# Kernel optimization log

Hardware: AMD Instinct MI355X
Metric: run time of the kernel (lower is better)

Reference implementation:

```python
import jax, jax.numpy as jnp
import numpy as np

NUM_EMBED = 1024
EMBED_DIM = 256
DECAY = 0.99
EPS = 1e-05
COMMIT = 0.25


def setup_inputs() -> dict:
    key = jax.random.key(0)
    k1, k2, k3 = jax.random.split(key, 3)
    z = jax.random.normal(k1, (64, 32, 32, EMBED_DIM), dtype=jnp.float32)
    lim = 1.0 / NUM_EMBED
    embeddings = jax.random.uniform(k2, (NUM_EMBED, EMBED_DIM), minval=-lim, maxval=lim, dtype=jnp.float32)
    ema_embed = jax.random.uniform(k3, (NUM_EMBED, EMBED_DIM), minval=-lim, maxval=lim, dtype=jnp.float32)
    cluster_size = jnp.zeros((NUM_EMBED,), dtype=jnp.float32)
    return {"z": z, "embeddings": embeddings, "ema_embed": ema_embed, "cluster_size": cluster_size}


def reference(z, embeddings, ema_embed, cluster_size):
    B, H, W, D = z.shape
    zf = z.reshape(-1, D)  # [N, D]
    # squared euclidean distances to codebook: [N, K]
    distances = (zf ** 2).sum(-1, keepdims=True) + (embeddings ** 2).sum(-1) - 2.0 * (zf @ embeddings.T)
    closest = jnp.argmin(distances, axis=-1)  # [N] int
    quantized_indices = closest.reshape(B, H, W)[:, None]  # [B,1,H,W]
    quantized = embeddings[closest].reshape(z.shape)  # gather instead of one-hot GEMM

    # --- training-mode EMA codebook update (buffer math, no grads) ---
    n_i = jnp.zeros((NUM_EMBED,), dtype=zf.dtype).at[closest].add(1.0)  # per-code counts
    new_cluster = cluster_size * DECAY + n_i * (1.0 - DECAY)
    dw = jnp.zeros_like(embeddings).at[closest].add(zf)  # scatter-add of assigned vectors
    new_ema = ema_embed * DECAY + dw * (1.0 - DECAY)
    n = new_cluster.sum()
    new_cluster = (new_cluster + EPS) / (n + NUM_EMBED * EPS) * n
    new_embeddings = new_ema / new_cluster[:, None]

    commitment_loss = jnp.mean((quantized - z) ** 2)
    st_quantized = z + jax.lax.stop_gradient(quantized - z)  # straight-through
    loss = commitment_loss * COMMIT
    return loss, st_quantized, quantized_indices, new_embeddings, new_cluster, new_ema
```

## Files before the change

### kernel.cpp

```cpp
#include <hip/hip_runtime.h>
#include <float.h>
#include <stdint.h>

#define K_EMB 1024
#define D_EMB 256

typedef _Float16 half8 __attribute__((ext_vector_type(8)));
typedef float f32x4_t __attribute__((ext_vector_type(4)));

typedef const __attribute__((address_space(1))) void* as1cv;
typedef __attribute__((address_space(3))) void* as3v;


__global__ void convert_e_kernel(const float* __restrict__ e, _Float16* __restrict__ ehp,
                                 float* __restrict__ t2, unsigned int* __restrict__ flag_cnt) {
  if (blockIdx.x == 0 && threadIdx.x == 0) { flag_cnt[0] = 0; flag_cnt[1] = 0; }
  int row = blockIdx.x * 4 + (threadIdx.x >> 6);
  int lane = threadIdx.x & 63;
  float4 v = ((const float4*)(e + (size_t)row * D_EMB))[lane];
  float s = v.x * v.x + v.y * v.y + v.z * v.z + v.w * v.w;
#pragma unroll
  for (int off = 32; off > 0; off >>= 1) s += __shfl_down(s, off, 64);
  if (lane == 0) t2[row] = s;
  _Float16* dst = ehp + (size_t)row * D_EMB + lane * 4;
  dst[0] = (_Float16)v.x; dst[1] = (_Float16)v.y;
  dst[2] = (_Float16)v.z; dst[3] = (_Float16)v.w;
}


#define BM 128
#define CCH 32
#define NCH (K_EMB / CCH)
#define DELTA 1.5e-4f

__launch_bounds__(256, 3)
__global__ void argmin_mfma_kernel(const float* __restrict__ z,
                                   const _Float16* __restrict__ eh,
                                   const float* __restrict__ t2,
                                   int* __restrict__ closest,
                                   float* __restrict__ idx_out,
                                   unsigned int* __restrict__ flag_cnt,
                                   unsigned int* __restrict__ flag_row,
                                   unsigned int* __restrict__ flag_cand) {
  __shared__ _Float16 ebuf[3][CCH * D_EMB];
  const int tid = threadIdx.x;
  const int wid = tid >> 6;
  const int lane = tid & 63;
  const int c = lane & 15, g = lane >> 4;
  const int row0 = blockIdx.x * BM + wid * 32;

  half8 A[2][8];
#pragma unroll
  for (int fr = 0; fr < 2; ++fr)
#pragma unroll
    for (int df = 0; df < 8; ++df) {
      const float* zp = z + (size_t)(row0 + fr * 16 + c) * D_EMB + df * 32 + g * 8;
      const float4 v0 = *(const float4*)zp;
      const float4 v1 = *(const float4*)(zp + 4);
      half8 h;
      h[0] = (_Float16)v0.x; h[1] = (_Float16)v0.y; h[2] = (_Float16)v0.z; h[3] = (_Float16)v0.w;
      h[4] = (_Float16)v1.x; h[5] = (_Float16)v1.y; h[6] = (_Float16)v1.z; h[7] = (_Float16)v1.w;
      A[fr][df] = h;
    }

  float m1[8], m2[8], m3[8];
  int k1[8], k2[8];
#pragma unroll
  for (int s = 0; s < 8; ++s) { m1[s] = FLT_MAX; m2[s] = FLT_MAX; m3[s] = FLT_MAX; k1[s] = 0; k2[s] = 0; }

#define INS(s, dvv, kkv)                                        \
  {                                                             \
    const float dv_ = (dvv); const int kk_ = (kkv);             \
    const bool lt1 = dv_ < m1[s];                               \
    const bool lt2 = dv_ < m2[s];                               \
    m3[s] = __builtin_amdgcn_fmed3f(m2[s], m3[s], dv_);         \
    const float nm2 = __builtin_amdgcn_fmed3f(m1[s], m2[s], dv_); \
    k2[s] = lt1 ? k1[s] : (lt2 ? kk_ : k2[s]);                  \
    m2[s] = nm2;                                                \
    m1[s] = fminf(m1[s], dv_);                                  \
    k1[s] = lt1 ? kk_ : k1[s];                                  \
  }

  const int rswz = (c & 7) << 3;

  int sgs[4];
#pragma unroll
  for (int u = 0; u < 4; ++u) {
    const int gidx = (wid * 4 + u) * 64 + lane;
    sgs[u] = (gidx & ~7) | ((gidx & 7) ^ ((gidx >> 5) & 7));
  }

#define ISSUE(cbn, buf)                                                              \
  {                                                                                  \
    const _Float16* src_ = eh + (size_t)(cbn) * (CCH * D_EMB);                       \
    _Float16* db_ = &ebuf[buf][0];                                                   \
    _Pragma("unroll")                                                                \
    for (int u = 0; u < 4; ++u)                                                      \
      __builtin_amdgcn_global_load_lds((as1cv)(src_ + (size_t)sgs[u] * 8),           \
                                       (as3v)(db_ + (wid * 4 + u) * 512), 16, 0, 0); \
  }

#define COMPUTE(rb_, cb_)                                                            \
  {                                                                                  \
    f32x4_t acc[2][2];                                                               \
    _Pragma("unroll")                                                                \
    for (int fr = 0; fr < 2; ++fr)                                                   \
      _Pragma("unroll")                                                              \
      for (int fc = 0; fc < 2; ++fc) acc[fr][fc] = (f32x4_t){0.f, 0.f, 0.f, 0.f};    \
    _Pragma("unroll")                                                                \
    for (int d = 0; d < 8; ++d) {                                                    \
      half8 Bh[2];                                                                   \
      _Pragma("unroll")                                                              \
      for (int fc = 0; fc < 2; ++fc) {                                               \
        const int elem = (d * 32 + g * 8) ^ rswz;                                    \
        Bh[fc] = *(const half8*)(&ebuf[rb_][(fc * 16 + c) * D_EMB + elem]);          \
      }                                                                              \
      _Pragma("unroll")                                                              \
      for (int fr = 0; fr < 2; ++fr)                                                 \
        _Pragma("unroll")                                                            \
        for (int fc = 0; fc < 2; ++fc)                                               \
          acc[fr][fc] = __builtin_amdgcn_mfma_f32_16x16x32_f16(A[fr][d], Bh[fc],     \
                                                               acc[fr][fc], 0, 0, 0);\
    }                                                                                \
    _Pragma("unroll")                                                                \
    for (int fc = 0; fc < 2; ++fc) {                                                 \
      const int kk = (cb_)*CCH + fc * 16 + c;                                        \
      const float t2c = t2[kk];                                                      \
      _Pragma("unroll")                                                              \
      for (int fr = 0; fr < 2; ++fr)                                                 \
        _Pragma("unroll")                                                            \
        for (int r = 0; r < 4; ++r) {                                                \
          const float dv = fmaf(-2.f, acc[fr][fc][r], t2c);                          \
          const int s = fr * 4 + r;                                                  \
          INS(s, dv, kk)                                                             \
        }                                                                            \
    }                                                                                \
  }

  ISSUE(0, 0)
  ISSUE(1, 1)

  for (int cb = 0; cb < NCH - 1; ++cb) {
    asm volatile("s_waitcnt vmcnt(4)" ::: "memory");
    __builtin_amdgcn_s_barrier();
    __builtin_amdgcn_sched_barrier(0);
    if (cb + 2 < NCH) ISSUE(cb + 2, (cb + 2) % 3)
    const int rb = cb % 3;
    COMPUTE(rb, cb)
  }
  asm volatile("s_waitcnt vmcnt(0)" ::: "memory");
  __builtin_amdgcn_s_barrier();
  __builtin_amdgcn_sched_barrier(0);
  {
    const int rb = (NCH - 1) % 3;
    COMPUTE(rb, NCH - 1)
  }
#undef COMPUTE
#undef ISSUE

#pragma unroll
  for (int m = 1; m <= 8; m <<= 1) {
#pragma unroll
    for (int s = 0; s < 8; ++s) {
      const float om1 = __shfl_xor(m1[s], m, 64);
      const int ok1 = __shfl_xor(k1[s], m, 64);
      const float om2 = __shfl_xor(m2[s], m, 64);
      const int ok2 = __shfl_xor(k2[s], m, 64);
      const float om3 = __shfl_xor(m3[s], m, 64);
      INS(s, om1, ok1)
      INS(s, om2, ok2)
      m3[s] = fminf(m3[s], om3);
    }
  }
#undef INS

  if (c == 0) {
#pragma unroll
    for (int s = 0; s < 8; ++s) {
      const int fr = s >> 2, r = s & 3;
      const int row = row0 + fr * 16 + g * 4 + r;
      closest[row] = k1[s];
      idx_out[row] = (float)k1[s];
      if (m2[s] - m1[s] < DELTA) {
        const unsigned int p = atomicAdd(flag_cnt, 1u);
        flag_row[p] = (unsigned int)row;
        flag_cand[p] = (unsigned int)k1[s] | ((unsigned int)k2[s] << 10) |
                       ((m3[s] - m1[s] < DELTA) ? (1u << 20) : 0u);
      }
    }
  }
}


__launch_bounds__(256, 4)
__global__ void fixup_pair_kernel(const float* __restrict__ z, const float* __restrict__ emb,
                                  const float* __restrict__ t2,
                                  const unsigned int* __restrict__ flag_cnt,
                                  const unsigned int* __restrict__ flag_row,
                                  const unsigned int* __restrict__ flag_cand,
                                  int* __restrict__ closest, float* __restrict__ idx_out,
                                  unsigned int* __restrict__ flag2_cnt,
                                  unsigned int* __restrict__ flag2) {
  const int tid = threadIdx.x;
  const int q = tid & 3;
  const unsigned int cnt = *flag_cnt;
  const unsigned int nquads = (gridDim.x * 256) >> 2;
  for (unsigned int i = (blockIdx.x * 256 + tid) >> 2; i < cnt; i += nquads) {
    const int row = (int)flag_row[i];
    const unsigned int cand = flag_cand[i];
    if ((cand >> 20) & 1u) {
      if (q == 0) {
        const unsigned int p = atomicAdd(flag2_cnt, 1u);
        flag2[p] = (unsigned int)row;
      }
      continue;
    }
    const int ka = (int)(cand & 1023u), kb = (int)((cand >> 10) & 1023u);
    const float4* zp = (const float4*)(z + (size_t)row * D_EMB) + q * 16;
    const float4* ap = (const float4*)(emb + (size_t)ka * D_EMB) + q * 16;
    const float4* bp = (const float4*)(emb + (size_t)kb * D_EMB) + q * 16;
    float s0 = 0.f, sa = 0.f, sb = 0.f;
#pragma unroll 8
    for (int u = 0; u < 16; ++u) {
      const float4 zv = zp[u], av = ap[u], bv = bp[u];
      s0 = fmaf(zv.x, zv.x, s0); s0 = fmaf(zv.y, zv.y, s0);
      s0 = fmaf(zv.z, zv.z, s0); s0 = fmaf(zv.w, zv.w, s0);
      sa = fmaf(zv.x, av.x, sa); sa = fmaf(zv.y, av.y, sa);
      sa = fmaf(zv.z, av.z, sa); sa = fmaf(zv.w, av.w, sa);
      sb = fmaf(zv.x, bv.x, sb); sb = fmaf(zv.y, bv.y, sb);
      sb = fmaf(zv.z, bv.z, sb); sb = fmaf(zv.w, bv.w, sb);
    }
#pragma unroll
    for (int m = 1; m <= 2; m <<= 1) {
      s0 += __shfl_xor(s0, m, 64);
      sa += __shfl_xor(sa, m, 64);
      sb += __shfl_xor(sb, m, 64);
    }
    if (q == 0) {
      const float da = (s0 + t2[ka]) - 2.f * sa;
      const float db = (s0 + t2[kb]) - 2.f * sb;
      int kbest = ka;
      if (db < da || (db == da && kb < ka)) kbest = kb;
      closest[row] = kbest;
      idx_out[row] = (float)kbest;
    }
  }
}


__launch_bounds__(256, 4)
__global__ void fixup_full_kernel(const float* __restrict__ z, const float* __restrict__ emb,
                                  const float* __restrict__ t2,
                                  const unsigned int* __restrict__ flag2_cnt,
                                  const unsigned int* __restrict__ flag2,
                                  int* __restrict__ closest, float* __restrict__ idx_out) {
  __shared__ float zs[D_EMB];
  __shared__ float t1s;
  __shared__ float redm[4];
  __shared__ int redk[4];
  const int tid = threadIdx.x;
  const int lane = tid & 63, wv = tid >> 6;
  const unsigned int cnt = *flag2_cnt;
  for (unsigned int j = blockIdx.x; j < cnt; j += gridDim.x) {
    __syncthreads();
    const int row = (int)flag2[j];
    if (wv == 0) {
      const float4 v = ((const float4*)(z + (size_t)row * D_EMB))[lane];
      ((float4*)zs)[lane] = v;
      float s = v.x * v.x + v.y * v.y + v.z * v.z + v.w * v.w;
#pragma unroll
      for (int off = 32; off > 0; off >>= 1) s += __shfl_down(s, off, 64);
      if (lane == 0) t1s = s;
    }
    __syncthreads();
    const float4* e0 = (const float4*)(emb + (size_t)(4 * tid + 0) * D_EMB);
    const float4* e1 = (const float4*)(emb + (size_t)(4 * tid + 1) * D_EMB);
    const float4* e2 = (const float4*)(emb + (size_t)(4 * tid + 2) * D_EMB);
    const float4* e3 = (const float4*)(emb + (size_t)(4 * tid + 3) * D_EMB);
    const float4* zp4 = (const float4*)zs;
    float a0 = 0.f, a1 = 0.f, a2 = 0.f, a3 = 0.f;
    for (int i = 0; i < 64; ++i) {
      const float4 z4 = zp4[i];
      const float4 v0 = e0[i], v1 = e1[i], v2 = e2[i], v3 = e3[i];
      a0 = fmaf(z4.x, v0.x, a0); a0 = fmaf(z4.y, v0.y, a0);
      a0 = fmaf(z4.z, v0.z, a0); a0 = fmaf(z4.w, v0.w, a0);
      a1 = fmaf(z4.x, v1.x, a1); a1 = fmaf(z4.y, v1.y, a1);
      a1 = fmaf(z4.z, v1.z, a1); a1 = fmaf(z4.w, v1.w, a1);
      a2 = fmaf(z4.x, v2.x, a2); a2 = fmaf(z4.y, v2.y, a2);
      a2 = fmaf(z4.z, v2.z, a2); a2 = fmaf(z4.w, v2.w, a2);
      a3 = fmaf(z4.x, v3.x, a3); a3 = fmaf(z4.y, v3.y, a3);
      a3 = fmaf(z4.z, v3.z, a3); a3 = fmaf(z4.w, v3.w, a3);
    }
    const float t1v = t1s;
    float best = FLT_MAX;
    int bk = 0x7fffffff;
    const float dvs[4] = {(t1v + t2[4 * tid + 0]) - 2.f * a0,
                          (t1v + t2[4 * tid + 1]) - 2.f * a1,
                          (t1v + t2[4 * tid + 2]) - 2.f * a2,
                          (t1v + t2[4 * tid + 3]) - 2.f * a3};
#pragma unroll
    for (int cc = 0; cc < 4; ++cc) {
      const int k = 4 * tid + cc;
      if (dvs[cc] < best) { best = dvs[cc]; bk = k; }
    }
#pragma unroll
    for (int m = 1; m <= 32; m <<= 1) {
      const float ob = __shfl_xor(best, m, 64);
      const int ok = __shfl_xor(bk, m, 64);
      if (ob < best || (ob == best && ok < bk)) { best = ob; bk = ok; }
    }
    if (lane == 0) { redm[wv] = best; redk[wv] = bk; }
    __syncthreads();
    if (tid == 0) {
      float b = redm[0];
      int k = redk[0];
#pragma unroll
      for (int w = 1; w < 4; ++w)
        if (redm[w] < b || (redm[w] == b && redk[w] < k)) { b = redm[w]; k = redk[w]; }
      closest[row] = k;
      idx_out[row] = (float)k;
    }
  }
}


__global__ void hist1_kernel(const int* __restrict__ closest, unsigned int* __restrict__ rank,
                             unsigned int* __restrict__ blockhist) {
  __shared__ unsigned int lh[K_EMB];
  const int t = threadIdx.x;
  lh[t] = 0;
  __syncthreads();
  const int row = blockIdx.x * 1024 + t;
  rank[row] = atomicAdd(&lh[closest[row]], 1u);
  __syncthreads();
  blockhist[blockIdx.x * K_EMB + t] = lh[t];
}

__global__ void hist2_kernel(unsigned int* __restrict__ blockhist, const float* __restrict__ cs,
                             unsigned int* __restrict__ base, float* __restrict__ newc,
                             float* __restrict__ o_ncl, int nblocks) {
  __shared__ unsigned int sc[K_EMB];
  __shared__ float fr[K_EMB];
  const int bin = threadIdx.x;
  unsigned int s = 0;
  if (nblocks == 64) {
    unsigned int v[64];
#pragma unroll
    for (int b = 0; b < 64; ++b) v[b] = blockhist[b * K_EMB + bin];
#pragma unroll
    for (int b = 0; b < 64; ++b) { const unsigned int t = v[b]; blockhist[b * K_EMB + bin] = s; s += t; }
  } else {
    for (int b = 0; b < nblocks; ++b) {
      const unsigned int v = blockhist[b * K_EMB + bin];
      blockhist[b * K_EMB + bin] = s;
      s += v;
    }
  }
  sc[bin] = s;
  __syncthreads();
  for (int off = 1; off < K_EMB; off <<= 1) {
    const unsigned int t = (bin >= off) ? sc[bin - off] : 0u;
    __syncthreads();
    sc[bin] += t;
    __syncthreads();
  }
  base[bin] = sc[bin] - s;
  const float pre = cs[bin] * 0.99f + (float)s * (float)(1.0 - 0.99);
  fr[bin] = pre;
  __syncthreads();
  for (int st = 512; st > 0; st >>= 1) {
    if (bin < st) fr[bin] += fr[bin + st];
    __syncthreads();
  }
  const float n = fr[0];
  const float ncl = (pre + 1e-5f) / (n + (float)(K_EMB * 1e-5)) * n;
  newc[bin] = ncl;
  o_ncl[bin] = ncl;
}

__global__ void hist3_kernel(const int* __restrict__ closest, const unsigned int* __restrict__ rank,
                             const unsigned int* __restrict__ blockhist,
                             const unsigned int* __restrict__ base,
                             unsigned int* __restrict__ sorted) {
  const int t = threadIdx.x;
  const int row = blockIdx.x * 1024 + t;
  const int k = closest[row];
  sorted[base[k] + blockhist[blockIdx.x * K_EMB + k] + rank[row]] = (unsigned int)row;
}


__global__ void dwsum_kernel(const float* __restrict__ z, const unsigned int* __restrict__ sorted,
                             const unsigned int* __restrict__ base, const float* __restrict__ ema,
                             const float* __restrict__ newc, const float* __restrict__ emb,
                             float* __restrict__ o_st, float* __restrict__ o_nema,
                             float* __restrict__ o_nemb, float* __restrict__ loss_part, int N) {
  const int k = blockIdx.x;
  const int lane = threadIdx.x & 63, wv = threadIdx.x >> 6;
  const unsigned int b0 = base[k];
  const unsigned int b1 = (k == K_EMB - 1) ? (unsigned int)N : base[k + 1];
  const float4 ev = ((const float4*)(emb + (size_t)k * D_EMB))[lane];
  float4 acc = {0.f, 0.f, 0.f, 0.f};
  float ls = 0.f;
  for (unsigned int j = b0 + wv; j < b1; j += 4) {
    const unsigned int row = sorted[j];
    const float4 zv = ((const float4*)(z + (size_t)row * D_EMB))[lane];
    const float dx = ev.x - zv.x, dy = ev.y - zv.y, dz = ev.z - zv.z, dww = ev.w - zv.w;
    float* sp = o_st + (size_t)row * D_EMB + lane * 4;
    sp[0] = zv.x + dx; sp[1] = zv.y + dy; sp[2] = zv.z + dz; sp[3] = zv.w + dww;
    ls = fmaf(dx, dx, ls); ls = fmaf(dy, dy, ls);
    ls = fmaf(dz, dz, ls); ls = fmaf(dww, dww, ls);
    acc.x += zv.x; acc.y += zv.y; acc.z += zv.z; acc.w += zv.w;
  }
  __shared__ float4 red[256];
  __shared__ float lred[256];
  red[threadIdx.x] = acc;
  lred[threadIdx.x] = ls;
  __syncthreads();
  for (int s = 128; s > 0; s >>= 1) {
    if (threadIdx.x < s) lred[threadIdx.x] += lred[threadIdx.x + s];
    __syncthreads();
  }
  if (threadIdx.x == 0) loss_part[k] = lred[0];
  if (wv == 0) {
    const float4 a1 = red[64 + lane], a2 = red[128 + lane], a3 = red[192 + lane];
    acc = red[lane];
    acc.x += a1.x + a2.x + a3.x;
    acc.y += a1.y + a2.y + a3.y;
    acc.z += a1.z + a2.z + a3.z;
    acc.w += a1.w + a2.w + a3.w;
    const float4 emv = ((const float4*)ema)[k * 64 + lane];
    const float nc = newc[k];
    const int off = k * D_EMB + lane * 4;
    float ne;
    ne = emv.x * 0.99f + acc.x * (float)(1.0 - 0.99); o_nema[off + 0] = ne; o_nemb[off + 0] = ne / nc;
    ne = emv.y * 0.99f + acc.y * (float)(1.0 - 0.99); o_nema[off + 1] = ne; o_nemb[off + 1] = ne / nc;
    ne = emv.z * 0.99f + acc.z * (float)(1.0 - 0.99); o_nema[off + 2] = ne; o_nemb[off + 2] = ne / nc;
    ne = emv.w * 0.99f + acc.w * (float)(1.0 - 0.99); o_nema[off + 3] = ne; o_nemb[off + 3] = ne / nc;
  }
}

__global__ void loss_final_kernel(const float* __restrict__ loss_part,
                                  float* __restrict__ o_loss, int nrows) {
  const int i = threadIdx.x;
  __shared__ double dred[1024];
  dred[i] = (double)loss_part[i];
  __syncthreads();
  for (int s = 512; s > 0; s >>= 1) {
    if (i < s) dred[i] += dred[i + s];
    __syncthreads();
  }
  if (i == 0) o_loss[0] = (float)(0.25 * (dred[0] / ((double)nrows * (double)D_EMB)));
}


extern "C" void kernel_launch(void* const* d_in, const int* in_sizes, int n_in,
                              void* d_out, int out_size, void* d_ws, size_t ws_size,
                              hipStream_t stream) {
  const float* z = (const float*)d_in[0];
  const float* emb = (const float*)d_in[1];
  const float* ema = (const float*)d_in[2];
  const float* cs = (const float*)d_in[3];
  const int N = in_sizes[0] / D_EMB;
  const int NB = N / 1024;

  float* out = (float*)d_out;
  float* o_loss = out;
  float* o_st = out + 1;
  float* o_idx = o_st + (size_t)N * D_EMB;
  float* o_nemb = o_idx + N;
  float* o_ncl = o_nemb + (size_t)K_EMB * D_EMB;
  float* o_nema = o_ncl + K_EMB;

  float* ws = (float*)d_ws;
  float* t2 = ws;
  float* newc = t2 + K_EMB;
  float* loss_part = newc + K_EMB;
  unsigned int* flag_cnt = (unsigned int*)(loss_part + K_EMB);
  unsigned int* basep = flag_cnt + 4;
  _Float16* ehp = (_Float16*)(basep + K_EMB);
  int* closest = (int*)(ehp + (size_t)K_EMB * D_EMB);
  unsigned int* flag_row = (unsigned int*)(closest + N);
  unsigned int* flag_cand = flag_row + N;
  unsigned int* sorted = flag_cand + N;
  unsigned int* flag2 = sorted + N;

  unsigned int* rank = flag_row;
  unsigned int* blockhist = flag_cand;
  unsigned int* flag2_cnt = flag_cnt + 1;

  convert_e_kernel<<<K_EMB / 4, 256, 0, stream>>>(emb, ehp, t2, flag_cnt);
  argmin_mfma_kernel<<<N / BM, 256, 0, stream>>>(z, ehp, t2, closest, o_idx,
                                                 flag_cnt, flag_row, flag_cand);
  fixup_pair_kernel<<<128, 256, 0, stream>>>(z, emb, t2, flag_cnt, flag_row, flag_cand,
                                             closest, o_idx, flag2_cnt, flag2);
  fixup_full_kernel<<<128, 256, 0, stream>>>(z, emb, t2, flag2_cnt, flag2, closest, o_idx);
  hist1_kernel<<<NB, 1024, 0, stream>>>(closest, rank, blockhist);
  hist2_kernel<<<1, 1024, 0, stream>>>(blockhist, cs, basep, newc, o_ncl, NB);
  hist3_kernel<<<NB, 1024, 0, stream>>>(closest, rank, blockhist, basep, sorted);
  dwsum_kernel<<<K_EMB, 256, 0, stream>>>(z, sorted, basep, ema, newc, emb,
                                          o_st, o_nema, o_nemb, loss_part, N);
  loss_final_kernel<<<1, 1024, 0, stream>>>(loss_part, o_loss, N);
}
```

Baseline: 187.8 us.

## Software-pipeline MFMA with argmin fold and merge fixup kernels into one launch

The argmin loop now uses two accumulator sets and a 4-deep LDS ring, so the MFMA work for one codebook chunk can overlap the distance-fold/top-3 insertion of the previous chunk. The argmin kernel now sorts ambiguous rows straight into a pair list or a full-rescan list, which lets the two fixup kernels merge into a single launch with more blocks. The cost is more LDS per block (4 buffers), which may lower occupancy at the 3-block launch bound, and more accumulator registers.

```diff
diff --git a/kernel.cpp b/kernel.cpp
--- a/kernel.cpp
+++ b/kernel.cpp
@@ -41,8 +41,9 @@
                                    float* __restrict__ idx_out,
                                    unsigned int* __restrict__ flag_cnt,
                                    unsigned int* __restrict__ flag_row,
-                                   unsigned int* __restrict__ flag_cand) {
-  __shared__ _Float16 ebuf[3][CCH * D_EMB];
+                                   unsigned int* __restrict__ flag_cand,
+                                   unsigned int* __restrict__ flag2) {
+  __shared__ _Float16 ebuf[4][CCH * D_EMB];
   const int tid = threadIdx.x;
   const int wid = tid >> 6;
   const int lane = tid & 63;
@@ -100,13 +101,12 @@
                                        (as3v)(db_ + (wid * 4 + u) * 512), 16, 0, 0); \
   }
 
-#define COMPUTE(rb_, cb_)                                                            \
+#define MFMA_CHUNK(rb_, ACC)                                                         \
   {                                                                                  \
-    f32x4_t acc[2][2];                                                               \
     _Pragma("unroll")                                                                \
     for (int fr = 0; fr < 2; ++fr)                                                   \
       _Pragma("unroll")                                                              \
-      for (int fc = 0; fc < 2; ++fc) acc[fr][fc] = (f32x4_t){0.f, 0.f, 0.f, 0.f};    \
+      for (int fc = 0; fc < 2; ++fc) ACC[fr][fc] = (f32x4_t){0.f, 0.f, 0.f, 0.f};    \
     _Pragma("unroll")                                                                \
     for (int d = 0; d < 8; ++d) {                                                    \
       half8 Bh[2];                                                                   \
@@ -119,9 +119,13 @@
       for (int fr = 0; fr < 2; ++fr)                                                 \
         _Pragma("unroll")                                                            \
         for (int fc = 0; fc < 2; ++fc)                                               \
-          acc[fr][fc] = __builtin_amdgcn_mfma_f32_16x16x32_f16(A[fr][d], Bh[fc],     \
-                                                               acc[fr][fc], 0, 0, 0);\
+          ACC[fr][fc] = __builtin_amdgcn_mfma_f32_16x16x32_f16(A[fr][d], Bh[fc],     \
+                                                               ACC[fr][fc], 0, 0, 0);\
     }                                                                                \
+  }
+
+#define FOLD(ACC, cb_)                                                               \
+  {                                                                                  \
     _Pragma("unroll")                                                                \
     for (int fc = 0; fc < 2; ++fc) {                                                 \
       const int kk = (cb_)*CCH + fc * 16 + c;                                        \
@@ -130,32 +134,45 @@
       for (int fr = 0; fr < 2; ++fr)                                                 \
         _Pragma("unroll")                                                            \
         for (int r = 0; r < 4; ++r) {                                                \
-          const float dv = fmaf(-2.f, acc[fr][fc][r], t2c);                          \
+          const float dv = fmaf(-2.f, ACC[fr][fc][r], t2c);                          \
           const int s = fr * 4 + r;                                                  \
           INS(s, dv, kk)                                                             \
         }                                                                            \
     }                                                                                \
   }
 
+  f32x4_t accA[2][2], accB[2][2];
+
   ISSUE(0, 0)
   ISSUE(1, 1)
 
-  for (int cb = 0; cb < NCH - 1; ++cb) {
+  for (int cb = 0; cb < NCH - 2; cb += 2) {
     asm volatile("s_waitcnt vmcnt(4)" ::: "memory");
     __builtin_amdgcn_s_barrier();
     __builtin_amdgcn_sched_barrier(0);
-    if (cb + 2 < NCH) ISSUE(cb + 2, (cb + 2) % 3)
-    const int rb = cb % 3;
-    COMPUTE(rb, cb)
-  }
+    ISSUE(cb + 2, (cb + 2) & 3)
+    MFMA_CHUNK(cb & 3, accA)
+    if (cb) FOLD(accB, cb - 1)
+    asm volatile("s_waitcnt vmcnt(4)" ::: "memory");
+    __builtin_amdgcn_s_barrier();
+    __builtin_amdgcn_sched_barrier(0);
+    ISSUE(cb + 3, (cb + 3) & 3)
+    MFMA_CHUNK((cb + 1) & 3, accB)
+    FOLD(accA, cb)
+  }
+  asm volatile("s_waitcnt vmcnt(4)" ::: "memory");
+  __builtin_amdgcn_s_barrier();
+  __builtin_amdgcn_sched_barrier(0);
+  MFMA_CHUNK((NCH - 2) & 3, accA)
+  FOLD(accB, NCH - 3)
   asm volatile("s_waitcnt vmcnt(0)" ::: "memory");
   __builtin_amdgcn_s_barrier();
   __builtin_amdgcn_sched_barrier(0);
-  {
-    const int rb = (NCH - 1) % 3;
-    COMPUTE(rb, NCH - 1)
-  }
-#undef COMPUTE
+  MFMA_CHUNK((NCH - 1) & 3, accB)
+  FOLD(accA, NCH - 2)
+  FOLD(accB, NCH - 1)
+#undef MFMA_CHUNK
+#undef FOLD
 #undef ISSUE
 
 #pragma unroll
@@ -182,10 +199,14 @@
       closest[row] = k1[s];
       idx_out[row] = (float)k1[s];
       if (m2[s] - m1[s] < DELTA) {
-        const unsigned int p = atomicAdd(flag_cnt, 1u);
-        flag_row[p] = (unsigned int)row;
-        flag_cand[p] = (unsigned int)k1[s] | ((unsigned int)k2[s] << 10) |
-                       ((m3[s] - m1[s] < DELTA) ? (1u << 20) : 0u);
+        if (m3[s] - m1[s] < DELTA) {
+          const unsigned int p = atomicAdd(&flag_cnt[1], 1u);
+          flag2[p] = (unsigned int)row;
+        } else {
+          const unsigned int p = atomicAdd(&flag_cnt[0], 1u);
+          flag_row[p] = (unsigned int)row;
+          flag_cand[p] = (unsigned int)k1[s] | ((unsigned int)k2[s] << 10);
+        }
       }
     }
   }
@@ -193,75 +214,59 @@
 
 
 __launch_bounds__(256, 4)
-__global__ void fixup_pair_kernel(const float* __restrict__ z, const float* __restrict__ emb,
-                                  const float* __restrict__ t2,
-                                  const unsigned int* __restrict__ flag_cnt,
-                                  const unsigned int* __restrict__ flag_row,
-                                  const unsigned int* __restrict__ flag_cand,
-                                  int* __restrict__ closest, float* __restrict__ idx_out,
-                                  unsigned int* __restrict__ flag2_cnt,
-                                  unsigned int* __restrict__ flag2) {
+__global__ void fixup_kernel(const float* __restrict__ z, const float* __restrict__ emb,
+                             const float* __restrict__ t2,
+                             const unsigned int* __restrict__ flag_cnt,
+                             const unsigned int* __restrict__ flag1_row,
+                             const unsigned int* __restrict__ flag1_cand,
+                             const unsigned int* __restrict__ flag2,
+                             int* __restrict__ closest, float* __restrict__ idx_out) {
   const int tid = threadIdx.x;
-  const int q = tid & 3;
-  const unsigned int cnt = *flag_cnt;
-  const unsigned int nquads = (gridDim.x * 256) >> 2;
-  for (unsigned int i = (blockIdx.x * 256 + tid) >> 2; i < cnt; i += nquads) {
-    const int row = (int)flag_row[i];
-    const unsigned int cand = flag_cand[i];
-    if ((cand >> 20) & 1u) {
+  {
+    const int q = tid & 3;
+    const unsigned int cnt = flag_cnt[0];
+    const unsigned int nquads = (gridDim.x * 256) >> 2;
+    for (unsigned int i = (blockIdx.x * 256 + tid) >> 2; i < cnt; i += nquads) {
+      const int row = (int)flag1_row[i];
+      const unsigned int cand = flag1_cand[i];
+      const int ka = (int)(cand & 1023u), kb = (int)((cand >> 10) & 1023u);
+      const float4* zp = (const float4*)(z + (size_t)row * D_EMB) + q * 16;
+      const float4* ap = (const float4*)(emb + (size_t)ka * D_EMB) + q * 16;
+      const float4* bp = (const float4*)(emb + (size_t)kb * D_EMB) + q * 16;
+      float s0 = 0.f, sa = 0.f, sb = 0.f;
+#pragma unroll 8
+      for (int u = 0; u < 16; ++u) {
+        const float4 zv = zp[u], av = ap[u], bv = bp[u];
+        s0 = fmaf(zv.x, zv.x, s0); s0 = fmaf(zv.y, zv.y, s0);
+        s0 = fmaf(zv.z, zv.z, s0); s0 = fmaf(zv.w, zv.w, s0);
+        sa = fmaf(zv.x, av.x, sa); sa = fmaf(zv.y, av.y, sa);
+        sa = fmaf(zv.z, av.z, sa); sa = fmaf(zv.w, av.w, sa);
+        sb = fmaf(zv.x, bv.x, sb); sb = fmaf(zv.y, bv.y, sb);
+        sb = fmaf(zv.z, bv.z, sb); sb = fmaf(zv.w, bv.w, sb);
+      }
+#pragma unroll
+      for (int m = 1; m <= 2; m <<= 1) {
+        s0 += __shfl_xor(s0, m, 64);
+        sa += __shfl_xor(sa, m, 64);
+        sb += __shfl_xor(sb, m, 64);
+      }
       if (q == 0) {
-        const unsigned int p = atomicAdd(flag2_cnt, 1u);
-        flag2[p] = (unsigned int)row;
+        const float da = (s0 + t2[ka]) - 2.f * sa;
+        const float db = (s0 + t2[kb]) - 2.f * sb;
+        int kbest = ka;
+        if (db < da || (db == da && kb < ka)) kbest = kb;
+        closest[row] = kbest;
+        idx_out[row] = (float)kbest;
       }
-      continue;
-    }
-    const int ka = (int)(cand & 1023u), kb = (int)((cand >> 10) & 1023u);
-    const float4* zp = (const float4*)(z + (size_t)row * D_EMB) + q * 16;
-    const float4* ap = (const float4*)(emb + (size_t)ka * D_EMB) + q * 16;
-    const float4* bp = (const float4*)(emb + (size_t)kb * D_EMB) + q * 16;
-    float s0 = 0.f, sa = 0.f, sb = 0.f;
-#pragma unroll 8
-    for (int u = 0; u < 16; ++u) {
-      const float4 zv = zp[u], av = ap[u], bv = bp[u];
-      s0 = fmaf(zv.x, zv.x, s0); s0 = fmaf(zv.y, zv.y, s0);
-      s0 = fmaf(zv.z, zv.z, s0); s0 = fmaf(zv.w, zv.w, s0);
-      sa = fmaf(zv.x, av.x, sa); sa = fmaf(zv.y, av.y, sa);
-      sa = fmaf(zv.z, av.z, sa); sa = fmaf(zv.w, av.w, sa);
-      sb = fmaf(zv.x, bv.x, sb); sb = fmaf(zv.y, bv.y, sb);
-      sb = fmaf(zv.z, bv.z, sb); sb = fmaf(zv.w, bv.w, sb);
-    }
-#pragma unroll
-    for (int m = 1; m <= 2; m <<= 1) {
-      s0 += __shfl_xor(s0, m, 64);
-      sa += __shfl_xor(sa, m, 64);
-      sb += __shfl_xor(sb, m, 64);
-    }
-    if (q == 0) {
-      const float da = (s0 + t2[ka]) - 2.f * sa;
-      const float db = (s0 + t2[kb]) - 2.f * sb;
-      int kbest = ka;
-      if (db < da || (db == da && kb < ka)) kbest = kb;
-      closest[row] = kbest;
-      idx_out[row] = (float)kbest;
-    }
-  }
-}
-
-
-__launch_bounds__(256, 4)
-__global__ void fixup_full_kernel(const float* __restrict__ z, const float* __restrict__ emb,
-                                  const float* __restrict__ t2,
-                                  const unsigned int* __restrict__ flag2_cnt,
-                                  const unsigned int* __restrict__ flag2,
-                                  int* __restrict__ closest, float* __restrict__ idx_out) {
+    }
+  }
   __shared__ float zs[D_EMB];
   __shared__ float t1s;
   __shared__ float redm[4];
   __shared__ int redk[4];
-  const int tid = threadIdx.x;
   const int lane = tid & 63, wv = tid >> 6;
-  const unsigned int cnt = *flag2_cnt;
-  for (unsigned int j = blockIdx.x; j < cnt; j += gridDim.x) {
+  const unsigned int cnt2 = flag_cnt[1];
+  for (unsigned int j = blockIdx.x; j < cnt2; j += gridDim.x) {
     __syncthreads();
     const int row = (int)flag2[j];
     if (wv == 0) {
@@ -486,14 +491,12 @@
 
   unsigned int* rank = flag_row;
   unsigned int* blockhist = flag_cand;
-  unsigned int* flag2_cnt = flag_cnt + 1;
 
   convert_e_kernel<<<K_EMB / 4, 256, 0, stream>>>(emb, ehp, t2, flag_cnt);
   argmin_mfma_kernel<<<N / BM, 256, 0, stream>>>(z, ehp, t2, closest, o_idx,
-                                                 flag_cnt, flag_row, flag_cand);
-  fixup_pair_kernel<<<128, 256, 0, stream>>>(z, emb, t2, flag_cnt, flag_row, flag_cand,
-                                             closest, o_idx, flag2_cnt, flag2);
-  fixup_full_kernel<<<128, 256, 0, stream>>>(z, emb, t2, flag2_cnt, flag2, closest, o_idx);
+                                                 flag_cnt, flag_row, flag_cand, flag2);
+  fixup_kernel<<<256, 256, 0, stream>>>(z, emb, t2, flag_cnt, flag_row, flag_cand, flag2,
+                                        closest, o_idx);
   hist1_kernel<<<NB, 1024, 0, stream>>>(closest, rank, blockhist);
   hist2_kernel<<<1, 1024, 0, stream>>>(blockhist, cs, basep, newc, o_ncl, NB);
   hist3_kernel<<<NB, 1024, 0, stream>>>(closest, rank, blockhist, basep, sorted);
```

Result: faster. 179.7 us (-4.3%).
